# Performance work log

Measured on AMD Instinct MI355X. Metric: run time of the kernel, lower is better.

Reference implementation:

```python
import jax, jax.numpy as jnp
import numpy as np

TOP_P = 0.9


def _nucleus_filter(logits, top_p):
    """Top-p (nucleus) filtering, row-wise over the last axis.

    Faithful to the torch version: sort descending, cumsum of softmax,
    mask entries past top_p (shifted right by one so the first token
    always survives), scatter -inf back into original positions.
    logits: [S, V]
    """
    order = jnp.argsort(-logits, axis=-1)                      # [S, V] descending order
    sorted_logits = jnp.take_along_axis(logits, order, axis=-1)
    cum = jnp.cumsum(jax.nn.softmax(sorted_logits, axis=-1), axis=-1)
    remove = cum > top_p                                       # [S, V] in sorted order
    # shift right: sorted_indices_to_remove[...,1:] = [..., :-1]; [...,0] = 0
    remove = jnp.concatenate(
        [jnp.zeros_like(remove[..., :1]), remove[..., :-1]], axis=-1)
    inv = jnp.argsort(order, axis=-1)                          # inverse permutation
    remove_orig = jnp.take_along_axis(remove, inv, axis=-1)    # mask in original order
    return jnp.where(remove_orig, -jnp.inf, logits)


def setup_inputs() -> dict:
    key = jax.random.key(0)
    # [max_length, vocab] = per-decode-step logits (loop batched over steps)
    logits = jax.random.normal(key, (512, 50257), dtype=jnp.float32) * 4.0
    return {"logits": logits}


def reference(logits):
    filt = _nucleus_filter(logits, TOP_P)
    # probabilities, decoder_input = torch.max(filtered, dim=-1)
    all_scores = jnp.max(filt, axis=-1)       # [S] float
    all_tokens = jnp.argmax(filt, axis=-1)    # [S] int — greedy pick of surviving logits
    return (all_tokens, all_scores)
```

## Files before the change

kernel.cpp:

```cpp
#include <hip/hip_runtime.h>
#include <hip/hip_bf16.h>
#include <stdint.h>
#include <math.h>


#define BLOCK 512

__global__ __launch_bounds__(BLOCK) void rowmax_argmax_kernel(
    const float* __restrict__ logits, float* __restrict__ out, int S, int V) {
    const int row = blockIdx.x;
    const float* rp = logits + (size_t)row * (size_t)V;

    int head = (int)(((16u - ((uintptr_t)rp & 15u)) & 15u) >> 2);
    if (head > V) head = V;
    const int nvec = (V - head) >> 2;
    const int tail_start = head + (nvec << 2);
    const int ntail = V - tail_start;

    const int tid = threadIdx.x;

    float best = -INFINITY;
    int bidx = 0x7fffffff;

    if (tid < head) {
        best = rp[tid];
        bidx = tid;
    }

    const float4* __restrict__ vp = (const float4*)(rp + head);
    for (int i = tid; i < nvec; i += BLOCK) {
        const float4 v = vp[i];
        const int base = head + (i << 2);
        if (v.x > best) { best = v.x; bidx = base; }
        if (v.y > best) { best = v.y; bidx = base + 1; }
        if (v.z > best) { best = v.z; bidx = base + 2; }
        if (v.w > best) { best = v.w; bidx = base + 3; }
    }

    if (tid < ntail) {
        const float v = rp[tail_start + tid];
        if (v > best) { best = v; bidx = tail_start + tid; }
    }

    #pragma unroll
    for (int off = 32; off >= 1; off >>= 1) {
        const float ov = __shfl_down(best, off, 64);
        const int   oi = __shfl_down(bidx, off, 64);
        if (ov > best || (ov == best && oi < bidx)) { best = ov; bidx = oi; }
    }

    __shared__ float s_val[BLOCK / 64];
    __shared__ int   s_idx[BLOCK / 64];
    const int wave = tid >> 6;
    const int lane = tid & 63;
    if (lane == 0) { s_val[wave] = best; s_idx[wave] = bidx; }
    __syncthreads();

    if (tid == 0) {
        float fb = s_val[0];
        int fi = s_idx[0];
        #pragma unroll
        for (int w = 1; w < BLOCK / 64; ++w) {
            const float ov = s_val[w];
            const int   oi = s_idx[w];
            if (ov > fb || (ov == fb && oi < fi)) { fb = ov; fi = oi; }
        }
        out[row]     = (float)fi;
        out[S + row] = fb;
    }
}

extern "C" void kernel_launch(void* const* d_in, const int* in_sizes, int n_in,
                              void* d_out, int out_size, void* d_ws, size_t ws_size,
                              hipStream_t stream) {
    const float* logits = (const float*)d_in[0];
    float* out = (float*)d_out;

    const int S = out_size / 2;
    const int V = in_sizes[0] / S;

    rowmax_argmax_kernel<<<S, BLOCK, 0, stream>>>(logits, out, S, V);
}
```

Before: 22.00 us.

## Split each row across four blocks with a merge pass and unrolled loads

The single block-per-row reduction becomes a two-kernel scheme. Each row is cut into four segments, each reduced by its own 256-thread block into a workspace of partial max/argmax pairs. A small second kernel merges the four partials per row. The inner loop now keeps four independent accumulators and issues four float4 loads per iteration, so more memory requests are in flight and the grid is four times larger. The cost is an extra kernel launch and a round trip through workspace memory.

Measured after the change: 23.23 us. 1.06x slower.

```diff
diff --git a/kernel.cpp b/kernel.cpp
--- a/kernel.cpp
+++ b/kernel.cpp
@@ -4,43 +4,81 @@
 #include <math.h>
 
 
-#define BLOCK 512
+#define P 4
+#define T1 256
 
-__global__ __launch_bounds__(BLOCK) void rowmax_argmax_kernel(
-    const float* __restrict__ logits, float* __restrict__ out, int S, int V) {
-    const int row = blockIdx.x;
-    const float* rp = logits + (size_t)row * (size_t)V;
+__global__ __launch_bounds__(T1) void partial_rowmax_kernel(
+    const float* __restrict__ logits, float* __restrict__ pval,
+    int* __restrict__ pidx, int S, int V, int seg) {
+    const int bid = blockIdx.x;
+    const int row = bid >> 2;
+    const int p   = bid & 3;
+    const int start = p * seg;
+    int end = start + seg;
+    if (end > V) end = V;
+    const int n = end - start;
+
+    const float* rp = logits + (size_t)row * (size_t)V + start;
 
     int head = (int)(((16u - ((uintptr_t)rp & 15u)) & 15u) >> 2);
-    if (head > V) head = V;
-    const int nvec = (V - head) >> 2;
+    if (head > n) head = n;
+    const int nvec = (n - head) >> 2;
     const int tail_start = head + (nvec << 2);
-    const int ntail = V - tail_start;
+    const int ntail = n - tail_start;
 
     const int tid = threadIdx.x;
 
-    float best = -INFINITY;
-    int bidx = 0x7fffffff;
+    float b0 = -INFINITY, b1 = -INFINITY, b2 = -INFINITY, b3 = -INFINITY;
+    int i0 = 0x7fffffff, i1 = 0x7fffffff, i2 = 0x7fffffff, i3 = 0x7fffffff;
 
-    if (tid < head) {
-        best = rp[tid];
-        bidx = tid;
+    if (tid < head) { b0 = rp[tid]; i0 = start + tid; }
+
+    const float4* __restrict__ vp = (const float4*)(rp + head);
+    const int gbase = start + head;
+    int i = tid;
+    for (; i + 3 * T1 < nvec; i += 4 * T1) {
+        const float4 a = vp[i];
+        const float4 b = vp[i + T1];
+        const float4 c = vp[i + 2 * T1];
+        const float4 d = vp[i + 3 * T1];
+        const int ka = gbase + (i << 2);
+        const int kb = gbase + ((i + T1) << 2);
+        const int kc = gbase + ((i + 2 * T1) << 2);
+        const int kd = gbase + ((i + 3 * T1) << 2);
+        if (a.x > b0) { b0 = a.x; i0 = ka; }
+        if (a.y > b0) { b0 = a.y; i0 = ka + 1; }
+        if (a.z > b0) { b0 = a.z; i0 = ka + 2; }
+        if (a.w > b0) { b0 = a.w; i0 = ka + 3; }
+        if (b.x > b1) { b1 = b.x; i1 = kb; }
+        if (b.y > b1) { b1 = b.y; i1 = kb + 1; }
+        if (b.z > b1) { b1 = b.z; i1 = kb + 2; }
+        if (b.w > b1) { b1 = b.w; i1 = kb + 3; }
+        if (c.x > b2) { b2 = c.x; i2 = kc; }
+        if (c.y > b2) { b2 = c.y; i2 = kc + 1; }
+        if (c.z > b2) { b2 = c.z; i2 = kc + 2; }
+        if (c.w > b2) { b2 = c.w; i2 = kc + 3; }
+        if (d.x > b3) { b3 = d.x; i3 = kd; }
+        if (d.y > b3) { b3 = d.y; i3 = kd + 1; }
+        if (d.z > b3) { b3 = d.z; i3 = kd + 2; }
+        if (d.w > b3) { b3 = d.w; i3 = kd + 3; }
+    }
+    for (; i < nvec; i += T1) {
+        const float4 a = vp[i];
+        const int ka = gbase + (i << 2);
+        if (a.x > b0) { b0 = a.x; i0 = ka; }
+        if (a.y > b0) { b0 = a.y; i0 = ka + 1; }
+        if (a.z > b0) { b0 = a.z; i0 = ka + 2; }
+        if (a.w > b0) { b0 = a.w; i0 = ka + 3; }
+    }
+    if (tid < ntail) {
+        const float v = rp[tail_start + tid];
+        if (v > b0) { b0 = v; i0 = start + tail_start + tid; }
     }
 
-    const float4* __restrict__ vp = (const float4*)(rp + head);
-    for (int i = tid; i < nvec; i += BLOCK) {
-        const float4 v = vp[i];
-        const int base = head + (i << 2);
-        if (v.x > best) { best = v.x; bidx = base; }
-        if (v.y > best) { best = v.y; bidx = base + 1; }
-        if (v.z > best) { best = v.z; bidx = base + 2; }
-        if (v.w > best) { best = v.w; bidx = base + 3; }
-    }
-
-    if (tid < ntail) {
-        const float v = rp[tail_start + tid];
-        if (v > best) { best = v; bidx = tail_start + tid; }
-    }
+    float best = b0; int bidx = i0;
+    if (b1 > best || (b1 == best && i1 < bidx)) { best = b1; bidx = i1; }
+    if (b2 > best || (b2 == best && i2 < bidx)) { best = b2; bidx = i2; }
+    if (b3 > best || (b3 == best && i3 < bidx)) { best = b3; bidx = i3; }
 
     #pragma unroll
     for (int off = 32; off >= 1; off >>= 1) {
@@ -49,8 +87,8 @@
         if (ov > best || (ov == best && oi < bidx)) { best = ov; bidx = oi; }
     }
 
-    __shared__ float s_val[BLOCK / 64];
-    __shared__ int   s_idx[BLOCK / 64];
+    __shared__ float s_val[T1 / 64];
+    __shared__ int   s_idx[T1 / 64];
     const int wave = tid >> 6;
     const int lane = tid & 63;
     if (lane == 0) { s_val[wave] = best; s_idx[wave] = bidx; }
@@ -60,14 +98,31 @@
         float fb = s_val[0];
         int fi = s_idx[0];
         #pragma unroll
-        for (int w = 1; w < BLOCK / 64; ++w) {
+        for (int w = 1; w < T1 / 64; ++w) {
             const float ov = s_val[w];
             const int   oi = s_idx[w];
             if (ov > fb || (ov == fb && oi < fi)) { fb = ov; fi = oi; }
         }
-        out[row]     = (float)fi;
-        out[S + row] = fb;
+        pval[bid] = fb;
+        pidx[bid] = fi;
     }
+}
+
+__global__ __launch_bounds__(256) void final_merge_kernel(
+    const float* __restrict__ pval, const int* __restrict__ pidx,
+    float* __restrict__ out, int S) {
+    const int r = blockIdx.x * blockDim.x + threadIdx.x;
+    if (r >= S) return;
+    float best = pval[r * P];
+    int bidx = pidx[r * P];
+    #pragma unroll
+    for (int p = 1; p < P; ++p) {
+        const float v = pval[r * P + p];
+        const int   ix = pidx[r * P + p];
+        if (v > best || (v == best && ix < bidx)) { best = v; bidx = ix; }
+    }
+    out[r]     = (float)bidx;
+    out[S + r] = best;
 }
 
 extern "C" void kernel_launch(void* const* d_in, const int* in_sizes, int n_in,
@@ -78,6 +133,11 @@
 
     const int S = out_size / 2;
     const int V = in_sizes[0] / S;
+    const int seg = (V + P - 1) / P;
 
-    rowmax_argmax_kernel<<<S, BLOCK, 0, stream>>>(logits, out, S, V);
+    float* pval = (float*)d_ws;
+    int*   pidx = (int*)((char*)d_ws + (size_t)S * P * sizeof(float));
+
+    partial_rowmax_kernel<<<S * P, T1, 0, stream>>>(logits, pval, pidx, S, V, seg);
+    final_merge_kernel<<<(S + 255) / 256, 256, 0, stream>>>(pval, pidx, out, S);
 }
```
